# Kernel optimization log

Measured on AMD Instinct MI355X. Metric: run time of the kernel, lower is better.

## Reference

```python
import jax, jax.numpy as jnp
import numpy as np

# Hamilton product tables: out component q uses weight IDX[q,p] with sign SGN[q,p]
# applied to input component p. Components order: (r, i, j, k); weights order: (rr, ri, rj, rk).
IDX = np.array([[0, 1, 2, 3], [1, 0, 3, 2], [2, 3, 0, 1], [3, 2, 1, 0]])
SGN = np.array([[1., -1., -1., -1.], [1., 1., 1., -1.], [1., -1., 1., 1.], [1., 1., -1., 1.]], dtype=np.float32)


def _qlinear(x4, w, b):
    # x4: (B, 4, Cin4, H, W); w: (4, Cout4, Cin4); b: (4, Cout4)
    # Quaternion 1x1 conv == channel-mixing matmul with Hamilton sign structure.
    wstk = jnp.asarray(SGN)[:, :, None, None] * w[IDX]  # (4,4,Cout4,Cin4)
    out = jnp.einsum('qpoc,bpchw->bqohw', wstk, x4)
    return out + b[None, :, :, None, None]


def _qdwconv(x4, w, b):
    # x4: (B, 4, Cc, H, W); w: (4, Cc, 1, 3, 3) depthwise per-channel; b: (4, Cc)
    Cc = x4.shape[2]
    comps = [x4[:, p] for p in range(4)]  # each (B, Cc, H, W)
    outs = []
    for qc in range(4):
        acc = None
        for p in range(4):
            c = SGN[qc, p] * jax.lax.conv_general_dilated(
                comps[p], w[IDX[qc, p]], window_strides=(1, 1), padding='SAME',
                feature_group_count=Cc, dimension_numbers=('NCHW', 'OIHW', 'NCHW'))
            acc = c if acc is None else acc + c
        outs.append(acc + b[qc][None, :, None, None])
    return jnp.stack(outs, axis=1)  # (B, 4, Cc, H, W)


def setup_inputs() -> dict:
    key = jax.random.key(0)
    ks = jax.random.split(key, 4)
    B, Cc, H, W = 8, 256, 32, 32   # dim = 4*Cc = 1024
    dim = 4 * Cc
    num_heads, key_dim = 8, 128
    h = 3 * num_heads * key_dim    # 3072 total -> 768 per component
    x = jax.random.normal(ks[0], (B, Cc, 4, H, W), jnp.float32)
    w_qkv = jax.random.normal(ks[1], (4, h // 4, dim // 4), jnp.float32) * (1.0 / np.sqrt(dim))
    b_qkv = jnp.zeros((4, h // 4), jnp.float32)
    w_proj = jax.random.normal(ks[2], (4, dim // 4, dim // 4), jnp.float32) * (1.0 / np.sqrt(dim))
    b_proj = jnp.zeros((4, dim // 4), jnp.float32)
    w_pe = jax.random.normal(ks[3], (4, dim // 4, 1, 3, 3), jnp.float32) * (1.0 / 6.0)
    b_pe = jnp.zeros((4, dim // 4), jnp.float32)
    return {'x': x, 'w_qkv': w_qkv, 'b_qkv': b_qkv, 'w_proj': w_proj,
            'b_proj': b_proj, 'w_pe': w_pe, 'b_pe': b_pe}


def reference(x, w_qkv, b_qkv, w_proj, b_proj, w_pe, b_pe):
    B, Cc, Q, H, W = x.shape
    num_heads, key_dim = 8, 128
    scale = key_dim ** -0.5
    N = H * W
    xq = jnp.transpose(x, (0, 2, 1, 3, 4))            # (B, 4, Cc, H, W)
    qkv = _qlinear(xq, w_qkv, b_qkv)                  # (B, 4, 768, H, W)
    q4, k4, v4 = jnp.split(qkv, 3, axis=2)            # each (B, 4, 256, H, W)

    def to_heads(t):  # (B,4,Cc,H,W) -> (B, heads, key_dim, N)
        return t.reshape(B, 4 * Cc, N).reshape(B, num_heads, key_dim, N)

    q, k, v = to_heads(q4), to_heads(k4), to_heads(v4)
    scores = jnp.einsum('bhdn,bhdm->bhnm', q, k) * scale   # (B,H,N,N) fully materialized
    attn = jax.nn.softmax(scores, axis=-1)
    out = jnp.einsum('bhnm,bhdm->bhdn', attn, v)           # (B,H,key_dim,N)
    out4 = out.reshape(B, 4, Cc, H, W)
    out = _qlinear(out4, w_proj, b_proj) + _qdwconv(xq, w_pe, b_pe)
    return jnp.transpose(out, (0, 2, 1, 3, 4))             # (B, Cc, 4, H, W)
```

## Files before the change

kernel.cpp:

```cpp
#include <hip/hip_runtime.h>
#include <hip/hip_bf16.h>

typedef unsigned short u16;
typedef float f32x4 __attribute__((ext_vector_type(4)));
typedef __bf16 bf16x8 __attribute__((ext_vector_type(8)));
typedef unsigned short su8v __attribute__((ext_vector_type(8)));
typedef unsigned short su4v __attribute__((ext_vector_type(4)));

#define BB 8
#define NHD 8
#define DD 128
#define NN 1024
#define DIM 1024
#define H3 3072
#define MM 8192
#define QSC (0.08838834764831845f * 1.4426950408889634f)

__constant__ int   d_IDX[16] = {0,1,2,3, 1,0,3,2, 2,3,0,1, 3,2,1,0};
__constant__ float d_SGN[16] = {1.f,-1.f,-1.f,-1.f, 1.f,1.f,1.f,-1.f,
                                1.f,-1.f,1.f,1.f,  1.f,1.f,-1.f,1.f};

__device__ __forceinline__ f32x4 mfma16(su8v a, su8v b, f32x4 c) {
  return __builtin_amdgcn_mfma_f32_16x16x32_bf16(
      __builtin_bit_cast(bf16x8, a), __builtin_bit_cast(bf16x8, b), c, 0, 0, 0);
}
__device__ __forceinline__ u16 f2b(float f) {
  unsigned int u = __builtin_bit_cast(unsigned int, f);
  u += 0x7fffu + ((u >> 16) & 1u);
  return (u16)(u >> 16);
}
__device__ __forceinline__ float b2f(u16 v) {
  unsigned int u = ((unsigned int)v) << 16;
  return __builtin_bit_cast(float, u);
}
typedef const __attribute__((address_space(1))) unsigned int* gas_t;
typedef __attribute__((address_space(3))) unsigned int* las_t;
__device__ __forceinline__ void gll16(const u16* g, u16* l) {
  __builtin_amdgcn_global_load_lds((gas_t)g, (las_t)l, 16, 0, 0);
}

__global__ __launch_bounds__(256) void prep_weff(
    const float* __restrict__ wqkv, const float* __restrict__ wproj,
    u16* __restrict__ weffQ, u16* __restrict__ weffP) {
  int tid = blockIdx.x * 256 + threadIdx.x;
  int stride = gridDim.x * 256;
  for (int i = tid; i < H3 * DIM; i += stride) {
    int row = i >> 10, col = i & 1023;
    int q = row / 768, o = row - q * 768;
    int p = col >> 8, c = col & 255;
    float v = d_SGN[q * 4 + p] * wqkv[(d_IDX[q * 4 + p] * 768 + o) * 256 + c];
    if (o < 256) v *= QSC;
    weffQ[i] = f2b(v);
  }
  for (int i = tid; i < DIM * DIM; i += stride) {
    int row = i >> 10, col = i & 1023;
    int q = row >> 8, o = row & 255;
    int p = col >> 8, c = col & 255;
    weffP[i] = f2b(d_SGN[q * 4 + p] * wproj[(d_IDX[q * 4 + p] * 256 + o) * 256 + c]);
  }
}

__global__ __launch_bounds__(256) void prep_x(
    const float* __restrict__ x, u16* __restrict__ Ax) {
  __shared__ u16 T[64 * 264];
  int blk = blockIdx.x;
  int nc = blk & 15;
  int cc = (blk >> 4) & 3;
  int b = blk >> 6;
  int n0 = nc * 64, c0 = cc * 64;
  int tid = threadIdx.x;
  int nseg = tid & 15, rq = tid >> 4;
#pragma unroll
  for (int pass = 0; pass < 16; ++pass) {
    int rr = pass * 16 + rq;
    int p = rr >> 6, c = rr & 63;
    float4 f = *(const float4*)(x + (((size_t)(b * 256 + c0 + c)) * 4 + p) * 1024 +
                                n0 + nseg * 4);
    T[(nseg * 4 + 0) * 264 + rr] = f2b(f.x);
    T[(nseg * 4 + 1) * 264 + rr] = f2b(f.y);
    T[(nseg * 4 + 2) * 264 + rr] = f2b(f.z);
    T[(nseg * 4 + 3) * 264 + rr] = f2b(f.w);
  }
  __syncthreads();
  int nl = tid >> 5, lc = tid & 31;
#pragma unroll
  for (int pass = 0; pass < 8; ++pass) {
    int n = pass * 8 + nl;
    su8v v = *(const su8v*)(&T[n * 264 + lc * 8]);
    int pcl = lc * 8;
    *(su8v*)(Ax + (size_t)(b * 1024 + n0 + n) * 1024 + (pcl >> 6) * 256 + c0 +
             (pcl & 63)) = v;
  }
}

template <int BM, int BN>
__device__ __forceinline__ void gemm_core8(
    const u16* __restrict__ Ag, const u16* __restrict__ Bg,
    u16* As, u16* Bs, int tid, f32x4 (&acc)[4][4]) {
  constexpr int WN = BN / 64;
  constexpr int AC = BM / 64;
  constexpr int BC = BN / 64;
  constexpr int NT = 16;
  int w = tid >> 6, lane = tid & 63, l16 = lane & 15, quad = lane >> 4;
  int wm = w / WN, wn = w % WN;
  int x7 = l16 & 7;
  int srow = lane >> 3;
  int sblk = (lane & 7) ^ srow;

  auto STAGE_A = [&](int tt, int bs) {
#pragma unroll
    for (int c = 0; c < AC; ++c) {
      int r0 = c * 64 + w * 8;
      gll16(Ag + (size_t)(r0 + srow) * 1024 + tt * 64 + sblk * 8,
            As + (size_t)bs * (BM * 64) + r0 * 64);
    }
  };
  auto STAGE_B = [&](int tt, int bs) {
#pragma unroll
    for (int c = 0; c < BC; ++c) {
      int r0 = c * 64 + w * 8;
      gll16(Bg + (size_t)(r0 + srow) * 1024 + tt * 64 + sblk * 8,
            Bs + (size_t)bs * (BN * 64) + r0 * 64);
    }
  };

  STAGE_A(0, 0); STAGE_B(0, 0);
  STAGE_A(1, 1); STAGE_B(1, 1);
  asm volatile("s_waitcnt vmcnt(6)" ::: "memory");
  __builtin_amdgcn_s_barrier();

  int cur = 0, nxt = 1, stg = 2;
  for (int t = 0; t < NT; ++t) {
    const u16* At = As + (size_t)cur * (BM * 64);
    const u16* Bt = Bs + (size_t)cur * (BN * 64);
#pragma unroll
    for (int kk = 0; kk < 2; ++kk) {
      su8v af[4], bf[4];
#pragma unroll
      for (int i = 0; i < 4; ++i)
        af[i] = *(const su8v*)(At + (wm * 64 + i * 16 + l16) * 64 +
                               ((kk * 4 + quad) ^ x7) * 8);
#pragma unroll
      for (int j = 0; j < 4; ++j)
        bf[j] = *(const su8v*)(Bt + (wn * 64 + j * 16 + l16) * 64 +
                               ((kk * 4 + quad) ^ x7) * 8);
      if (t + 2 < NT) {
        if (kk == 0) STAGE_A(t + 2, stg);
        else         STAGE_B(t + 2, stg);
      }
      __builtin_amdgcn_s_setprio(1);
#pragma unroll
      for (int i = 0; i < 4; ++i)
#pragma unroll
        for (int j = 0; j < 4; ++j)
          acc[i][j] = mfma16(af[i], bf[j], acc[i][j]);
      __builtin_amdgcn_s_setprio(0);
    }
    if (t < NT - 2)       asm volatile("s_waitcnt vmcnt(6)" ::: "memory");
    else if (t == NT - 2) asm volatile("s_waitcnt vmcnt(0)" ::: "memory");
    asm volatile("" ::: "memory");
    __builtin_amdgcn_s_barrier();
    asm volatile("" ::: "memory");
    int tmp = cur; cur = nxt; nxt = stg; stg = tmp;
  }
}

__global__ __launch_bounds__(512, 2) void gemm_qkv_mfma(
    const u16* __restrict__ Ax, const u16* __restrict__ weffQ,
    const float* __restrict__ bqkv,
    u16* __restrict__ Qb, u16* __restrict__ Kb, u16* __restrict__ VbT) {
  __shared__ u16 smem[3 * 384 * 64];
  int bn0 = blockIdx.x * 256;
  int col0 = blockIdx.y * 128;
  int q = col0 / 768;
  int off = col0 - q * 768;
  int sel = off >> 8;
  int head = (q * 256 + (off & 255)) >> 7;
  int tid = threadIdx.x;
  int w = tid >> 6, lane = tid & 63, l16 = lane & 15, quad = lane >> 4;
  f32x4 acc[4][4];
#pragma unroll
  for (int i = 0; i < 4; ++i)
#pragma unroll
    for (int j = 0; j < 4; ++j) acc[i][j] = (f32x4){0.f, 0.f, 0.f, 0.f};

  if (sel == 2) {
    gemm_core8<256, 128>(Ax + (size_t)bn0 * 1024, weffQ + (size_t)col0 * 1024,
                         smem, smem + 3 * 256 * 64, tid, acc);
    int wm = w >> 1, wn = w & 1;
#pragma unroll
    for (int j = 0; j < 4; ++j) {
      int dl = wn * 64 + j * 16 + l16;
      float bias = bqkv[col0 + dl];
#pragma unroll
      for (int i = 0; i < 4; ++i) {
        int m = bn0 + wm * 64 + i * 16 + quad * 4;
        int b = m >> 10, npos = m & 1023;
        int bh = b * NHD + head;
        su4v pk;
#pragma unroll
        for (int r = 0; r < 4; ++r) pk[r] = f2b(acc[i][j][r] + bias);
        *(su4v*)(VbT + ((size_t)bh * DD + dl) * NN + npos) = pk;
      }
    }
  } else {
    gemm_core8<128, 256>(weffQ + (size_t)col0 * 1024, Ax + (size_t)bn0 * 1024,
                         smem, smem + 3 * 128 * 64, tid, acc);
    int wm = w >> 2, wn = w & 3;
    u16* dst = (sel == 0) ? Qb : Kb;
    float sc = (sel == 0) ? (float)QSC : 1.0f;
#pragma unroll
    for (int i = 0; i < 4; ++i) {
      int dbase = wm * 64 + i * 16 + quad * 4;
      float4 b4 = *(const float4*)(bqkv + col0 + dbase);
#pragma unroll
      for (int j = 0; j < 4; ++j) {
        int n = bn0 + wn * 64 + j * 16 + l16;
        int b = n >> 10, npos = n & 1023;
        int bh = b * NHD + head;
        su4v pk;
        pk[0] = f2b(acc[i][j][0] + b4.x * sc);
        pk[1] = f2b(acc[i][j][1] + b4.y * sc);
        pk[2] = f2b(acc[i][j][2] + b4.z * sc);
        pk[3] = f2b(acc[i][j][3] + b4.w * sc);
        *(su4v*)(dst + ((size_t)bh * NN + npos) * DD + dbase) = pk;
      }
    }
  }
}

__global__ __launch_bounds__(256) void attn_mfma(
    const u16* __restrict__ Qb, const u16* __restrict__ Kb,
    const u16* __restrict__ VbT, u16* __restrict__ OP,
    float* __restrict__ LS) {
  __shared__ u16 Ks[2][64 * 128];
  __shared__ u16 Vt[2][128 * 64];
  __shared__ u16 Ps[4 * 32 * 64];
  int blk = blockIdx.x;
  int bh = blk & 63;
  int rest = blk >> 6;
  int qt = rest & 7;
  int half = rest >> 3;
  int n0 = qt * 128;
  int tid = threadIdx.x;
  int w = tid >> 6, lane = tid & 63, l16 = lane & 15, quad = lane >> 4;
  const u16* Qg = Qb + ((size_t)bh * NN + n0) * DD;
  const u16* Kg = Kb + (size_t)bh * NN * DD;
  const u16* Vg = VbT + (size_t)bh * DD * NN;
  u16* Pw = Ps + w * 32 * 64;
  int x7 = l16 & 7;

  auto STAGE = [&](int kt, int s) {
    int c0 = half * 512 + kt * 64;
#pragma unroll
    for (int t = 0; t < 4; ++t) {
      int ci = w * 4 + t;
      int krow = ci * 4 + (lane >> 4);
      int kblk = (lane & 15) ^ (krow & 7);
      gll16(Kg + (size_t)(c0 + krow) * DD + kblk * 8, &Ks[s][ci * 512]);
      int dv = ci * 8 + (lane >> 3);
      int vblk = (lane & 7) ^ (dv & 7);
      gll16(Vg + (size_t)dv * NN + c0 + vblk * 8, &Vt[s][ci * 512]);
    }
  };

  su8v qreg[2][4];
#pragma unroll
  for (int mi = 0; mi < 2; ++mi)
#pragma unroll
    for (int ch = 0; ch < 4; ++ch)
      qreg[mi][ch] = *(const su8v*)(Qg + (size_t)(w * 32 + mi * 16 + l16) * DD +
                                    ch * 32 + quad * 8);

  float ls[2] = {0.f, 0.f};
  f32x4 accO[2][8];
#pragma unroll
  for (int mi = 0; mi < 2; ++mi)
#pragma unroll
    for (int dt = 0; dt < 8; ++dt) accO[mi][dt] = (f32x4){0.f, 0.f, 0.f, 0.f};

  STAGE(0, 0);
  asm volatile("s_waitcnt vmcnt(0)" ::: "memory");
  __builtin_amdgcn_s_barrier();

  for (int kt = 0; kt < 8; ++kt) {
    int s = kt & 1;
    if (kt + 1 < 8) STAGE(kt + 1, s ^ 1);

    f32x4 sacc[2][4];
#pragma unroll
    for (int mi = 0; mi < 2; ++mi)
#pragma unroll
      for (int j = 0; j < 4; ++j) sacc[mi][j] = (f32x4){0.f, 0.f, 0.f, 0.f};
#pragma unroll
    for (int j = 0; j < 4; ++j) {
#pragma unroll
      for (int ch = 0; ch < 4; ++ch) {
        su8v kf = *(const su8v*)(&Ks[s][(j * 16 + l16) * 128 +
                                        (((ch * 4 + quad) ^ x7) * 8)]);
        __builtin_amdgcn_s_setprio(1);
        sacc[0][j] = mfma16(kf, qreg[0][ch], sacc[0][j]);
        sacc[1][j] = mfma16(kf, qreg[1][ch], sacc[1][j]);
        __builtin_amdgcn_s_setprio(0);
      }
    }

#pragma unroll
    for (int mi = 0; mi < 2; ++mi)
#pragma unroll
      for (int j = 0; j < 4; ++j) {
        su4v pk;
#pragma unroll
        for (int r = 0; r < 4; ++r) {
          float p = __builtin_exp2f(sacc[mi][j][r]);
          ls[mi] += p;
          pk[r] = (u16)(__builtin_bit_cast(unsigned int, p) >> 16);
        }
        *(su4v*)(Pw + (mi * 16 + l16) * 64 +
                 (((j * 2 + (quad >> 1)) ^ x7) << 3) + (quad & 1) * 4) = pk;
      }

#pragma unroll
    for (int ch = 0; ch < 2; ++ch) {
      su8v pf0 = *(const su8v*)(Pw + l16 * 64 + (((ch * 4 + quad) ^ x7) << 3));
      su8v pf1 = *(const su8v*)(Pw + (16 + l16) * 64 +
                                (((ch * 4 + quad) ^ x7) << 3));
#pragma unroll
      for (int dt = 0; dt < 8; ++dt) {
        su8v vf = *(const su8v*)(&Vt[s][(dt * 16 + l16) * 64 +
                                        (((ch * 4 + quad) ^ x7) * 8)]);
        __builtin_amdgcn_s_setprio(1);
        accO[0][dt] = mfma16(pf0, vf, accO[0][dt]);
        accO[1][dt] = mfma16(pf1, vf, accO[1][dt]);
        __builtin_amdgcn_s_setprio(0);
      }
    }

    if (kt + 1 < 8) {
      asm volatile("s_waitcnt vmcnt(0)" ::: "memory");
      asm volatile("" ::: "memory");
      __builtin_amdgcn_s_barrier();
      asm volatile("" ::: "memory");
    }
  }

#pragma unroll
  for (int mi = 0; mi < 2; ++mi) {
    float s = ls[mi];
    s += __shfl_xor(s, 16, 64);
    s += __shfl_xor(s, 32, 64);
    ls[mi] = s;
  }
  size_t hb = (size_t)(half * 64 + bh);
  if (quad == 0) {
#pragma unroll
    for (int mi = 0; mi < 2; ++mi)
      LS[hb * NN + n0 + w * 32 + mi * 16 + l16] = ls[mi];
  }
#pragma unroll
  for (int mi = 0; mi < 2; ++mi)
#pragma unroll
    for (int r = 0; r < 4; ++r) {
      int row = w * 32 + mi * 16 + quad * 4 + r;
      size_t base = (hb * NN + n0 + row) * DD;
#pragma unroll
      for (int dt = 0; dt < 8; ++dt)
        OP[base + dt * 16 + l16] = f2b(accO[mi][dt][r]);
    }
}

__global__ __launch_bounds__(256) void attn_merge(
    const u16* __restrict__ OP, const float* __restrict__ LS,
    u16* __restrict__ AO) {
  size_t idx = (size_t)blockIdx.x * 256 + threadIdx.x;
  size_t e = idx * 4;
  int d = (int)(e & 127);
  size_t bhn = e >> 7;
  su4v a = *(const su4v*)(OP + bhn * DD + d);
  su4v b = *(const su4v*)(OP + (size_t)64 * NN * DD + bhn * DD + d);
  float inv = 1.0f / (LS[bhn] + LS[bhn + 64 * NN]);
  int bh = (int)(bhn >> 10), n = (int)(bhn & 1023);
  int bb = bh >> 3, head = bh & 7;
  su4v o;
#pragma unroll
  for (int r = 0; r < 4; ++r) o[r] = f2b((b2f(a[r]) + b2f(b[r])) * inv);
  *(su4v*)(AO + ((size_t)(bb * 1024 + n) * 1024) + head * 128 + d) = o;
}

__global__ __launch_bounds__(256) void qdwconv_kernel(
    const float* __restrict__ x, const float* __restrict__ wpe,
    const float* __restrict__ bpe, float* __restrict__ pe) {
  int blk = blockIdx.x;
  int co = blk & 255;
  int b = blk >> 8;
  __shared__ float pl[4][34 * 34];
  __shared__ float wsm[4][9];
  int tid = threadIdx.x;
  for (int i = tid; i < 4 * 34 * 34; i += 256) ((float*)pl)[i] = 0.f;
  if (tid < 36) wsm[tid / 9][tid % 9] = wpe[((tid / 9) * 256 + co) * 9 + tid % 9];
  __syncthreads();
  for (int i = tid; i < 4 * 1024; i += 256) {
    int p = i >> 10, n = i & 1023;
    int h = n >> 5, ww = n & 31;
    pl[p][(h + 1) * 34 + (ww + 1)] =
        x[(((size_t)b * 256 + co) * 4 + p) * 1024 + n];
  }
  __syncthreads();
  for (int n = tid; n < 1024; n += 256) {
    int h = n >> 5, ww = n & 31;
    float in[4][9];
#pragma unroll
    for (int p = 0; p < 4; ++p)
#pragma unroll
      for (int t = 0; t < 9; ++t)
        in[p][t] = pl[p][(h + t / 3) * 34 + (ww + t % 3)];
#pragma unroll
    for (int q = 0; q < 4; ++q) {
      float acc = bpe[q * 256 + co];
#pragma unroll
      for (int p = 0; p < 4; ++p) {
        int idx = d_IDX[q * 4 + p];
        float s = d_SGN[q * 4 + p];
        float sub = 0.f;
#pragma unroll
        for (int t = 0; t < 9; ++t) sub += in[p][t] * wsm[idx][t];
        acc += s * sub;
      }
      pe[(((size_t)b * 256 + co) * 4 + q) * 1024 + n] = acc;
    }
  }
}

__global__ __launch_bounds__(512, 2) void gemm_proj_mfma(
    const u16* __restrict__ AO, const u16* __restrict__ weffP,
    const float* __restrict__ bproj, const float* __restrict__ pe,
    float* __restrict__ out) {
  __shared__ u16 smem[3 * 384 * 64];
  int n0 = blockIdx.x * 256;
  int m0 = blockIdx.y * 128;
  int tid = threadIdx.x;
  f32x4 acc[4][4];
#pragma unroll
  for (int i = 0; i < 4; ++i)
#pragma unroll
    for (int j = 0; j < 4; ++j) acc[i][j] = (f32x4){0.f, 0.f, 0.f, 0.f};
  gemm_core8<128, 256>(weffP + (size_t)m0 * 1024, AO + (size_t)n0 * 1024,
                       smem, smem + 3 * 128 * 64, tid, acc);

  int w = tid >> 6, lane = tid & 63, l16 = lane & 15, quad = lane >> 4;
  int wm = w >> 2, wn = w & 3;
#pragma unroll
  for (int i = 0; i < 4; ++i) {
#pragma unroll
    for (int r = 0; r < 4; ++r) {
      int mrow = m0 + wm * 64 + i * 16 + quad * 4 + r;
      int q = mrow >> 8, o = mrow & 255;
      float bias = bproj[mrow];
#pragma unroll
      for (int j = 0; j < 4; ++j) {
        int n = n0 + wn * 64 + j * 16 + l16;
        int b = n >> 10, npos = n & 1023;
        size_t oidx = (((size_t)b * 256 + o) * 4 + q) * 1024 + npos;
        out[oidx] = pe[oidx] + acc[i][j][r] + bias;
      }
    }
  }
}

extern "C" void kernel_launch(void* const* d_in, const int* in_sizes, int n_in,
                              void* d_out, int out_size, void* d_ws,
                              size_t ws_size, hipStream_t stream) {
  const float* x      = (const float*)d_in[0];
  const float* w_qkv  = (const float*)d_in[1];
  const float* b_qkv  = (const float*)d_in[2];
  const float* w_proj = (const float*)d_in[3];
  const float* b_proj = (const float*)d_in[4];
  const float* w_pe   = (const float*)d_in[5];
  const float* b_pe   = (const float*)d_in[6];
  float* out = (float*)d_out;

  u16* ws = (u16*)d_ws;
  u16* weffQ = ws;
  u16* weffP = weffQ + (size_t)H3 * DIM;
  u16* Ax    = weffP + (size_t)DIM * DIM;
  u16* Qb    = Ax + (size_t)MM * DIM;
  u16* Kb    = Qb + (size_t)BB * NHD * NN * DD;
  u16* VbT   = Kb + (size_t)BB * NHD * NN * DD;
  u16* AO    = VbT + (size_t)BB * NHD * DD * NN;
  float* PE  = (float*)(AO + (size_t)MM * DIM);
  u16* OP    = (u16*)(PE + (size_t)MM * DIM);
  float* LS  = (float*)(OP + (size_t)2 * 64 * NN * DD);

  hipLaunchKernelGGL(prep_weff, dim3(4096), dim3(256), 0, stream,
                     w_qkv, w_proj, weffQ, weffP);
  hipLaunchKernelGGL(prep_x, dim3(512), dim3(256), 0, stream, x, Ax);
  hipLaunchKernelGGL(gemm_qkv_mfma, dim3(MM / 256, H3 / 128), dim3(512), 0,
                     stream, Ax, weffQ, b_qkv, Qb, Kb, VbT);
  hipLaunchKernelGGL(attn_mfma, dim3(1024), dim3(256), 0, stream,
                     Qb, Kb, VbT, OP, LS);
  hipLaunchKernelGGL(attn_merge, dim3((64 * NN * DD) / (256 * 4)), dim3(256),
                     0, stream, OP, LS, AO);
  hipLaunchKernelGGL(qdwconv_kernel, dim3(BB * 256), dim3(256), 0, stream,
                     x, w_pe, b_pe, PE);
  hipLaunchKernelGGL(gemm_proj_mfma, dim3(MM / 256, DIM / 128), dim3(512), 0,
                     stream, AO, weffP, b_proj, PE, out);
}
```

Before: 324.2 us.

## Keep P in registers via 16x16x16 MFMA, single-buffer K/V LDS

The attention kernel now feeds the exponentiated score fragments straight from registers into a 16x16x16 bf16 MFMA for the PV product. This removes the per-wave P shared-memory round trip. K/V staging drops from double to single buffering with two syncthreads per tile, and launch bounds request four blocks per CU. The smaller LDS footprint is meant to raise occupancy, at the cost of losing load/compute overlap inside a block, issuing twice as many PV MFMAs, and dropping the setprio hints.

```diff
diff --git a/kernel.cpp b/kernel.cpp
--- a/kernel.cpp
+++ b/kernel.cpp
@@ -4,8 +4,10 @@
 typedef unsigned short u16;
 typedef float f32x4 __attribute__((ext_vector_type(4)));
 typedef __bf16 bf16x8 __attribute__((ext_vector_type(8)));
+typedef __bf16 bf16x4 __attribute__((ext_vector_type(4)));
 typedef unsigned short su8v __attribute__((ext_vector_type(8)));
 typedef unsigned short su4v __attribute__((ext_vector_type(4)));
+typedef short s16x4 __attribute__((ext_vector_type(4)));
 
 #define BB 8
 #define NHD 8
@@ -23,6 +25,19 @@
 __device__ __forceinline__ f32x4 mfma16(su8v a, su8v b, f32x4 c) {
   return __builtin_amdgcn_mfma_f32_16x16x32_bf16(
       __builtin_bit_cast(bf16x8, a), __builtin_bit_cast(bf16x8, b), c, 0, 0, 0);
+}
+__device__ __forceinline__ f32x4 mfma16h(su4v a, su4v b, f32x4 c) {
+#if __has_builtin(__builtin_amdgcn_mfma_f32_16x16x16_bf16)
+  return __builtin_amdgcn_mfma_f32_16x16x16_bf16(
+      __builtin_bit_cast(bf16x4, a), __builtin_bit_cast(bf16x4, b), c, 0, 0, 0);
+#elif __has_builtin(__builtin_amdgcn_mfma_f32_16x16x16bf16_1k)
+  return __builtin_amdgcn_mfma_f32_16x16x16bf16_1k(
+      __builtin_bit_cast(s16x4, a), __builtin_bit_cast(s16x4, b), c, 0, 0, 0);
+#else
+  f32x4 d = c;
+  asm("v_mfma_f32_16x16x16_bf16 %0, %1, %2, %0" : "+v"(d) : "v"(a), "v"(b));
+  return d;
+#endif
 }
 __device__ __forceinline__ u16 f2b(float f) {
   unsigned int u = __builtin_bit_cast(unsigned int, f);
@@ -229,13 +244,12 @@
   }
 }
 
-__global__ __launch_bounds__(256) void attn_mfma(
+__global__ __launch_bounds__(256, 4) void attn_mfma(
     const u16* __restrict__ Qb, const u16* __restrict__ Kb,
     const u16* __restrict__ VbT, u16* __restrict__ OP,
     float* __restrict__ LS) {
-  __shared__ u16 Ks[2][64 * 128];
-  __shared__ u16 Vt[2][128 * 64];
-  __shared__ u16 Ps[4 * 32 * 64];
+  __shared__ u16 Ks[64 * 128];
+  __shared__ u16 Vt[128 * 64];
   int blk = blockIdx.x;
   int bh = blk & 63;
   int rest = blk >> 6;
@@ -247,100 +261,74 @@
   const u16* Qg = Qb + ((size_t)bh * NN + n0) * DD;
   const u16* Kg = Kb + (size_t)bh * NN * DD;
   const u16* Vg = VbT + (size_t)bh * DD * NN;
-  u16* Pw = Ps + w * 32 * 64;
   int x7 = l16 & 7;
 
-  auto STAGE = [&](int kt, int s) {
+  su8v qreg[2][4];
+#pragma unroll
+  for (int mi = 0; mi < 2; ++mi)
+#pragma unroll
+    for (int ch = 0; ch < 4; ++ch)
+      qreg[mi][ch] = *(const su8v*)(Qg + (size_t)(w * 32 + mi * 16 + l16) * DD +
+                                    ch * 32 + quad * 8);
+
+  float ls[2] = {0.f, 0.f};
+  f32x4 accO[2][8];
+#pragma unroll
+  for (int mi = 0; mi < 2; ++mi)
+#pragma unroll
+    for (int dt = 0; dt < 8; ++dt) accO[mi][dt] = (f32x4){0.f, 0.f, 0.f, 0.f};
+
+  for (int kt = 0; kt < 8; ++kt) {
     int c0 = half * 512 + kt * 64;
+    __syncthreads();
 #pragma unroll
     for (int t = 0; t < 4; ++t) {
       int ci = w * 4 + t;
       int krow = ci * 4 + (lane >> 4);
       int kblk = (lane & 15) ^ (krow & 7);
-      gll16(Kg + (size_t)(c0 + krow) * DD + kblk * 8, &Ks[s][ci * 512]);
+      gll16(Kg + (size_t)(c0 + krow) * DD + kblk * 8, Ks + ci * 512);
       int dv = ci * 8 + (lane >> 3);
       int vblk = (lane & 7) ^ (dv & 7);
-      gll16(Vg + (size_t)dv * NN + c0 + vblk * 8, &Vt[s][ci * 512]);
-    }
-  };
-
-  su8v qreg[2][4];
-#pragma unroll
-  for (int mi = 0; mi < 2; ++mi)
-#pragma unroll
-    for (int ch = 0; ch < 4; ++ch)
-      qreg[mi][ch] = *(const su8v*)(Qg + (size_t)(w * 32 + mi * 16 + l16) * DD +
-                                    ch * 32 + quad * 8);
-
-  float ls[2] = {0.f, 0.f};
-  f32x4 accO[2][8];
-#pragma unroll
-  for (int mi = 0; mi < 2; ++mi)
-#pragma unroll
-    for (int dt = 0; dt < 8; ++dt) accO[mi][dt] = (f32x4){0.f, 0.f, 0.f, 0.f};
-
-  STAGE(0, 0);
-  asm volatile("s_waitcnt vmcnt(0)" ::: "memory");
-  __builtin_amdgcn_s_barrier();
-
-  for (int kt = 0; kt < 8; ++kt) {
-    int s = kt & 1;
-    if (kt + 1 < 8) STAGE(kt + 1, s ^ 1);
-
-    f32x4 sacc[2][4];
-#pragma unroll
-    for (int mi = 0; mi < 2; ++mi)
-#pragma unroll
-      for (int j = 0; j < 4; ++j) sacc[mi][j] = (f32x4){0.f, 0.f, 0.f, 0.f};
+      gll16(Vg + (size_t)dv * NN + c0 + vblk * 8, Vt + ci * 512);
+    }
+    __syncthreads();
+
+    su4v pk[2][4];
 #pragma unroll
     for (int j = 0; j < 4; ++j) {
+      f32x4 s0 = (f32x4){0.f, 0.f, 0.f, 0.f};
+      f32x4 s1 = (f32x4){0.f, 0.f, 0.f, 0.f};
 #pragma unroll
       for (int ch = 0; ch < 4; ++ch) {
-        su8v kf = *(const su8v*)(&Ks[s][(j * 16 + l16) * 128 +
-                                        (((ch * 4 + quad) ^ x7) * 8)]);
-        __builtin_amdgcn_s_setprio(1);
-        sacc[0][j] = mfma16(kf, qreg[0][ch], sacc[0][j]);
-        sacc[1][j] = mfma16(kf, qreg[1][ch], sacc[1][j]);
-        __builtin_amdgcn_s_setprio(0);
-      }
-    }
-
-#pragma unroll
-    for (int mi = 0; mi < 2; ++mi)
-#pragma unroll
-      for (int j = 0; j < 4; ++j) {
-        su4v pk;
-#pragma unroll
-        for (int r = 0; r < 4; ++r) {
-          float p = __builtin_exp2f(sacc[mi][j][r]);
-          ls[mi] += p;
-          pk[r] = (u16)(__builtin_bit_cast(unsigned int, p) >> 16);
-        }
-        *(su4v*)(Pw + (mi * 16 + l16) * 64 +
-                 (((j * 2 + (quad >> 1)) ^ x7) << 3) + (quad & 1) * 4) = pk;
-      }
-
-#pragma unroll
-    for (int ch = 0; ch < 2; ++ch) {
-      su8v pf0 = *(const su8v*)(Pw + l16 * 64 + (((ch * 4 + quad) ^ x7) << 3));
-      su8v pf1 = *(const su8v*)(Pw + (16 + l16) * 64 +
-                                (((ch * 4 + quad) ^ x7) << 3));
+        su8v kf = *(const su8v*)(Ks + (j * 16 + l16) * 128 +
+                                 (((ch * 4 + quad) ^ x7) * 8));
+        s0 = mfma16(kf, qreg[0][ch], s0);
+        s1 = mfma16(kf, qreg[1][ch], s1);
+      }
+      su4v p0, p1;
+#pragma unroll
+      for (int r = 0; r < 4; ++r) {
+        float pa = __builtin_exp2f(s0[r]);
+        ls[0] += pa;
+        p0[r] = (u16)(__builtin_bit_cast(unsigned int, pa) >> 16);
+        float pb = __builtin_exp2f(s1[r]);
+        ls[1] += pb;
+        p1[r] = (u16)(__builtin_bit_cast(unsigned int, pb) >> 16);
+      }
+      pk[0][j] = p0;
+      pk[1][j] = p1;
+    }
+
+#pragma unroll
+    for (int j = 0; j < 4; ++j) {
 #pragma unroll
       for (int dt = 0; dt < 8; ++dt) {
-        su8v vf = *(const su8v*)(&Vt[s][(dt * 16 + l16) * 64 +
-                                        (((ch * 4 + quad) ^ x7) * 8)]);
-        __builtin_amdgcn_s_setprio(1);
-        accO[0][dt] = mfma16(pf0, vf, accO[0][dt]);
-        accO[1][dt] = mfma16(pf1, vf, accO[1][dt]);
-        __builtin_amdgcn_s_setprio(0);
-      }
-    }
-
-    if (kt + 1 < 8) {
-      asm volatile("s_waitcnt vmcnt(0)" ::: "memory");
-      asm volatile("" ::: "memory");
-      __builtin_amdgcn_s_barrier();
-      asm volatile("" ::: "memory");
+        su4v vf = *(const su4v*)(Vt + (dt * 16 + l16) * 64 +
+                                 ((((j * 2 + (quad >> 1)) ^ x7) << 3) +
+                                  (quad & 1) * 4));
+        accO[0][dt] = mfma16h(pk[0][j], vf, accO[0][dt]);
+        accO[1][dt] = mfma16h(pk[1][j], vf, accO[1][dt]);
+      }
     }
   }
 
```

Measured after the change: 361.9 us. +11.6%, slower.
